# Kernel optimization log

Measured on AMD Instinct MI355X. Metric: run time of the kernel, lower is better.

Reference implementation:

```python
import jax, jax.numpy as jnp
import numpy as np

B, C, H, WID = 32, 64, 128, 128
K = 5            # co-occurrence bins (co_shape)
WH = 3           # spatial filter height/width (w_shape = (1,3,3), depth 1)
ACT_LO, ACT_HI = 0.0, 1.0  # actBounds


def setup_inputs() -> dict:
    key = jax.random.key(0)
    k1, k2, k3 = jax.random.split(key, 3)
    input_tensor = jax.random.uniform(k1, (B, C, H, WID), dtype=jnp.float32)
    # learned params: L ~ N(0, 0.1) of shape (k,k); W ~ N(0,0.1) of shape (d,h,w)
    L = 0.1 * jax.random.normal(k2, (K, K), dtype=jnp.float32)
    W = 0.1 * jax.random.normal(k3, (1, WH, WH), dtype=jnp.float32)
    return {"input_tensor": input_tensor, "W": W, "L": L}


def _quantize(x, k):
    # map activation in [ACT_LO, ACT_HI] to bin index in [0, k-1]
    b = jnp.floor((x - ACT_LO) / (ACT_HI - ACT_LO) * k)
    return jnp.clip(b, 0, k - 1).astype(jnp.int32)


def reference(input_tensor, W, L):
    """Co-occurrence layer:
    out[p] = sum_{q in 3x3 nbhd(p)} W[q-p] * L[bin(x[q]), bin(x[p])] * x[q]
    Out-of-bounds neighbors contribute 0 (zero pad => x[q]=0 kills the term),
    matching the precomputed neighbor_lookup_table boundary handling.
    """
    k = L.shape[0]
    pad = WH // 2
    bins = _quantize(input_tensor, k)                      # (B,C,H,W) int32
    xp = jnp.pad(input_tensor, ((0, 0), (0, 0), (pad, pad), (pad, pad)))
    bp = jnp.pad(bins, ((0, 0), (0, 0), (pad, pad), (pad, pad)))
    h, w = input_tensor.shape[2], input_tensor.shape[3]
    out = jnp.zeros_like(input_tensor)
    for dh in range(WH):                                   # tiny fixed 3x3 loop
        for dw in range(WH):
            xn = xp[:, :, dh:dh + h, dw:dw + w]            # shifted neighbor values
            bn = bp[:, :, dh:dh + h, dw:dw + w]            # shifted neighbor bins
            out = out + W[0, dh, dw] * L[bn, bins] * xn    # gather L + weighted acc
    return out
```

## Files before the change

### kernel.cpp

```cpp
#include <hip/hip_runtime.h>


namespace {
constexpr int H  = 128;
constexpr int WD = 128;
constexpr int PLANES = 32 * 64;
constexpr int ROWS_PER_BLOCK = 16;
constexpr int PX = 8;
constexpr int THREADS = ROWS_PER_BLOCK * (WD / PX);
constexpr int TILES = H / ROWS_PER_BLOCK;
}

__global__ __launch_bounds__(THREADS) void col_kernel(
    const float* __restrict__ x, const float* __restrict__ Wf,
    const float* __restrict__ Lf, float* __restrict__ out)
{
    __shared__ float WL[9 * 25];
    const int t = threadIdx.x;
    if (t < 225) WL[t] = Wf[t / 25] * Lf[t % 25];
    __syncthreads();

    const int plane = blockIdx.x >> 3;
    const int tile  = blockIdx.x & 7;
    const int row   = tile * ROWS_PER_BLOCK + (t >> 4);
    const int col0  = (t & 15) * PX;

    const float* xp = x + (size_t)plane * (H * WD);

    float win[3][PX + 2];
    #pragma unroll
    for (int dr = 0; dr < 3; ++dr) {
        const int rr = row + dr - 1;
        const bool vr = (rr >= 0) && (rr < H);
        const float* rp = xp + rr * WD + col0;
        float4 c0 = make_float4(0.f, 0.f, 0.f, 0.f);
        float4 c1 = make_float4(0.f, 0.f, 0.f, 0.f);
        float l = 0.f, r = 0.f;
        if (vr) {
            c0 = *(const float4*)rp;
            c1 = *(const float4*)(rp + 4);
            if (col0 > 0)       l = rp[-1];
            if (col0 < WD - PX) r = rp[PX];
        }
        win[dr][0] = l;
        win[dr][1] = c0.x; win[dr][2] = c0.y; win[dr][3] = c0.z; win[dr][4] = c0.w;
        win[dr][5] = c1.x; win[dr][6] = c1.y; win[dr][7] = c1.z; win[dr][8] = c1.w;
        win[dr][9] = r;
    }

    int bq20[3][PX + 2];
    int bp4[PX];
    #pragma unroll
    for (int dr = 0; dr < 3; ++dr) {
        #pragma unroll
        for (int j = 0; j < PX + 2; ++j) {
            int b = (int)(win[dr][j] * 5.0f);
            b = (b > 4) ? 4 : b;
            bq20[dr][j] = b * 20;
            if (dr == 1 && j >= 1 && j <= PX) bp4[j - 1] = b * 4;
        }
    }

    const char* wlb = (const char*)WL;
    float acc[PX];
    #pragma unroll
    for (int i = 0; i < PX; ++i) acc[i] = 0.f;

    #pragma unroll
    for (int dr = 0; dr < 3; ++dr) {
        #pragma unroll
        for (int dw = 0; dw < 3; ++dw) {
            #pragma unroll
            for (int i = 0; i < PX; ++i) {
                const float lw = *(const float*)(
                    wlb + (bq20[dr][i + dw] + bp4[i] + (dr * 3 + dw) * 100));
                acc[i] = fmaf(lw, win[dr][i + dw], acc[i]);
            }
        }
    }

    float* op = out + (size_t)plane * (H * WD) + row * WD + col0;
    *(float4*)op       = make_float4(acc[0], acc[1], acc[2], acc[3]);
    *(float4*)(op + 4) = make_float4(acc[4], acc[5], acc[6], acc[7]);
}

extern "C" void kernel_launch(void* const* d_in, const int* in_sizes, int n_in,
                              void* d_out, int out_size, void* d_ws, size_t ws_size,
                              hipStream_t stream) {
    const float* x  = (const float*)d_in[0];
    const float* Wf = (const float*)d_in[1];
    const float* Lf = (const float*)d_in[2];
    float* out = (float*)d_out;

    col_kernel<<<dim3(PLANES * TILES), dim3(THREADS), 0, stream>>>(x, Wf, Lf, out);
}
```

Baseline: 255.4 us.

## Compute two output rows per thread with shared window and nontemporal stores

Each thread now computes two vertically adjacent output rows, loading four input rows instead of three per row. This cuts redundant global loads of halo rows and the binning work per output. The block covers 32 rows, so each block handles a quarter plane, and launch bounds hint at 4 blocks per CU. Output writes use nontemporal vector stores to avoid polluting cache. The cost is more registers per thread, which may reduce occupancy.

```diff
diff --git a/kernel.cpp b/kernel.cpp
--- a/kernel.cpp
+++ b/kernel.cpp
@@ -5,13 +5,16 @@
 constexpr int H  = 128;
 constexpr int WD = 128;
 constexpr int PLANES = 32 * 64;
-constexpr int ROWS_PER_BLOCK = 16;
 constexpr int PX = 8;
-constexpr int THREADS = ROWS_PER_BLOCK * (WD / PX);
+constexpr int RPT = 2;
+constexpr int ROWS_PER_BLOCK = 32;
+constexpr int THREADS = (ROWS_PER_BLOCK / RPT) * (WD / PX);
 constexpr int TILES = H / ROWS_PER_BLOCK;
+
+typedef float vfloat4 __attribute__((ext_vector_type(4)));
 }
 
-__global__ __launch_bounds__(THREADS) void col_kernel(
+__global__ __launch_bounds__(THREADS, 4) void col_kernel(
     const float* __restrict__ x, const float* __restrict__ Wf,
     const float* __restrict__ Lf, float* __restrict__ out)
 {
@@ -20,17 +23,17 @@
     if (t < 225) WL[t] = Wf[t / 25] * Lf[t % 25];
     __syncthreads();
 
-    const int plane = blockIdx.x >> 3;
-    const int tile  = blockIdx.x & 7;
-    const int row   = tile * ROWS_PER_BLOCK + (t >> 4);
+    const int plane = blockIdx.x >> 2;
+    const int tile  = blockIdx.x & 3;
+    const int row0  = tile * ROWS_PER_BLOCK + (t >> 4) * RPT;
     const int col0  = (t & 15) * PX;
 
     const float* xp = x + (size_t)plane * (H * WD);
 
-    float win[3][PX + 2];
+    float win[4][PX + 2];
     #pragma unroll
-    for (int dr = 0; dr < 3; ++dr) {
-        const int rr = row + dr - 1;
+    for (int k = 0; k < 4; ++k) {
+        const int rr = row0 + k - 1;
         const bool vr = (rr >= 0) && (rr < H);
         const float* rp = xp + rr * WD + col0;
         float4 c0 = make_float4(0.f, 0.f, 0.f, 0.f);
@@ -42,46 +45,61 @@
             if (col0 > 0)       l = rp[-1];
             if (col0 < WD - PX) r = rp[PX];
         }
-        win[dr][0] = l;
-        win[dr][1] = c0.x; win[dr][2] = c0.y; win[dr][3] = c0.z; win[dr][4] = c0.w;
-        win[dr][5] = c1.x; win[dr][6] = c1.y; win[dr][7] = c1.z; win[dr][8] = c1.w;
-        win[dr][9] = r;
+        win[k][0] = l;
+        win[k][1] = c0.x; win[k][2] = c0.y; win[k][3] = c0.z; win[k][4] = c0.w;
+        win[k][5] = c1.x; win[k][6] = c1.y; win[k][7] = c1.z; win[k][8] = c1.w;
+        win[k][9] = r;
     }
 
-    int bq20[3][PX + 2];
-    int bp4[PX];
+    int bq20[4][PX + 2];
+    int bp4a[PX], bp4b[PX];
     #pragma unroll
-    for (int dr = 0; dr < 3; ++dr) {
+    for (int k = 0; k < 4; ++k) {
         #pragma unroll
         for (int j = 0; j < PX + 2; ++j) {
-            int b = (int)(win[dr][j] * 5.0f);
+            int b = (int)(win[k][j] * 5.0f);
             b = (b > 4) ? 4 : b;
-            bq20[dr][j] = b * 20;
-            if (dr == 1 && j >= 1 && j <= PX) bp4[j - 1] = b * 4;
+            bq20[k][j] = b * 20;
+            if (k == 1 && j >= 1 && j <= PX) bp4a[j - 1] = b * 4;
+            if (k == 2 && j >= 1 && j <= PX) bp4b[j - 1] = b * 4;
         }
     }
 
     const char* wlb = (const char*)WL;
-    float acc[PX];
+    float acca[PX], accb[PX];
     #pragma unroll
-    for (int i = 0; i < PX; ++i) acc[i] = 0.f;
+    for (int i = 0; i < PX; ++i) { acca[i] = 0.f; accb[i] = 0.f; }
 
     #pragma unroll
     for (int dr = 0; dr < 3; ++dr) {
         #pragma unroll
         for (int dw = 0; dw < 3; ++dw) {
+            const int imm = (dr * 3 + dw) * 100;
+            float lwa[PX], lwb[PX];
             #pragma unroll
-            for (int i = 0; i < PX; ++i) {
-                const float lw = *(const float*)(
-                    wlb + (bq20[dr][i + dw] + bp4[i] + (dr * 3 + dw) * 100));
-                acc[i] = fmaf(lw, win[dr][i + dw], acc[i]);
-            }
+            for (int i = 0; i < PX; ++i)
+                lwa[i] = *(const float*)(wlb + (bq20[dr][i + dw] + bp4a[i] + imm));
+            #pragma unroll
+            for (int i = 0; i < PX; ++i)
+                lwb[i] = *(const float*)(wlb + (bq20[dr + 1][i + dw] + bp4b[i] + imm));
+            #pragma unroll
+            for (int i = 0; i < PX; ++i)
+                acca[i] = fmaf(lwa[i], win[dr][i + dw], acca[i]);
+            #pragma unroll
+            for (int i = 0; i < PX; ++i)
+                accb[i] = fmaf(lwb[i], win[dr + 1][i + dw], accb[i]);
         }
     }
 
-    float* op = out + (size_t)plane * (H * WD) + row * WD + col0;
-    *(float4*)op       = make_float4(acc[0], acc[1], acc[2], acc[3]);
-    *(float4*)(op + 4) = make_float4(acc[4], acc[5], acc[6], acc[7]);
+    float* op = out + (size_t)plane * (H * WD) + row0 * WD + col0;
+    vfloat4 sa0 = { acca[0], acca[1], acca[2], acca[3] };
+    vfloat4 sa1 = { acca[4], acca[5], acca[6], acca[7] };
+    vfloat4 sb0 = { accb[0], accb[1], accb[2], accb[3] };
+    vfloat4 sb1 = { accb[4], accb[5], accb[6], accb[7] };
+    __builtin_nontemporal_store(sa0, (vfloat4*)op);
+    __builtin_nontemporal_store(sa1, (vfloat4*)(op + 4));
+    __builtin_nontemporal_store(sb0, (vfloat4*)(op + WD));
+    __builtin_nontemporal_store(sb1, (vfloat4*)(op + WD + 4));
 }
 
 extern "C" void kernel_launch(void* const* d_in, const int* in_sizes, int n_in,
```

New measurement: 245.4 us. 3.9% less time.

## Process eight rows per thread with a rolling register window and one block per plane

Applied to the files above, without the earlier changes.

Each block now covers a whole 128x128 plane, and each thread computes an 8-row by 8-column strip, so the grid shrinks from one block per 16-row tile to one block per plane. A rolling 4-row register window is kept and reused across output row pairs, with the next two rows prefetched before each compute step. This cuts redundant halo row loads and quantization from 3 rows per output row to about 1.25. The trade-offs are higher register pressure (launch bounds ask for 2 blocks per CU), fewer blocks to spread across the GPU, and a multiply-shift trick that derives bin*4 from bin*20.

```diff
diff --git a/kernel.cpp b/kernel.cpp
--- a/kernel.cpp
+++ b/kernel.cpp
@@ -5,13 +5,11 @@
 constexpr int H  = 128;
 constexpr int WD = 128;
 constexpr int PLANES = 32 * 64;
-constexpr int ROWS_PER_BLOCK = 16;
 constexpr int PX = 8;
-constexpr int THREADS = ROWS_PER_BLOCK * (WD / PX);
-constexpr int TILES = H / ROWS_PER_BLOCK;
+constexpr int THREADS = 256;
 }
 
-__global__ __launch_bounds__(THREADS) void col_kernel(
+__global__ __launch_bounds__(THREADS, 2) void col_kernel(
     const float* __restrict__ x, const float* __restrict__ Wf,
     const float* __restrict__ Lf, float* __restrict__ out)
 {
@@ -20,68 +18,108 @@
     if (t < 225) WL[t] = Wf[t / 25] * Lf[t % 25];
     __syncthreads();
 
-    const int plane = blockIdx.x >> 3;
-    const int tile  = blockIdx.x & 7;
-    const int row   = tile * ROWS_PER_BLOCK + (t >> 4);
-    const int col0  = (t & 15) * PX;
+    const int col0 = (t & 15) * PX;
+    const int r0   = (t >> 4) * 8;
 
-    const float* xp = x + (size_t)plane * (H * WD);
+    const float* xp = x + (size_t)blockIdx.x * (H * WD);
+    float* opb      = out + (size_t)blockIdx.x * (H * WD);
+    const char* wlb = (const char*)WL;
 
-    float win[3][PX + 2];
-    #pragma unroll
-    for (int dr = 0; dr < 3; ++dr) {
-        const int rr = row + dr - 1;
-        const bool vr = (rr >= 0) && (rr < H);
-        const float* rp = xp + rr * WD + col0;
-        float4 c0 = make_float4(0.f, 0.f, 0.f, 0.f);
-        float4 c1 = make_float4(0.f, 0.f, 0.f, 0.f);
-        float l = 0.f, r = 0.f;
-        if (vr) {
-            c0 = *(const float4*)rp;
-            c1 = *(const float4*)(rp + 4);
-            if (col0 > 0)       l = rp[-1];
-            if (col0 < WD - PX) r = rp[PX];
-        }
-        win[dr][0] = l;
-        win[dr][1] = c0.x; win[dr][2] = c0.y; win[dr][3] = c0.z; win[dr][4] = c0.w;
-        win[dr][5] = c1.x; win[dr][6] = c1.y; win[dr][7] = c1.z; win[dr][8] = c1.w;
-        win[dr][9] = r;
+    float win[4][PX + 2];
+    int   bq[4][PX + 2];
+    float n0[PX + 2], n1[PX + 2];
+
+#define LOAD_ROW(DST, RR) {                                               \
+    const int _rr = (RR);                                                 \
+    if (_rr >= 0 && _rr < H) {                                            \
+        const float* _rp = xp + _rr * WD + col0;                          \
+        const float4 _c0 = *(const float4*)_rp;          \
+        const float4 _c1 = *(const float4*)(_rp + 4);                     \
+        DST[0] = (col0 > 0) ? _rp[-1] : 0.f;                              \
+        DST[1] = _c0.x; DST[2] = _c0.y; DST[3] = _c0.z; DST[4] = _c0.w;   \
+        DST[5] = _c1.x; DST[6] = _c1.y; DST[7] = _c1.z; DST[8] = _c1.w;   \
+        DST[9] = (col0 < WD - PX) ? _rp[PX] : 0.f;                        \
+    } else {                                                              \
+        _Pragma("unroll")                                                 \
+        for (int _j = 0; _j < PX + 2; ++_j) DST[_j] = 0.f;                \
+    } }
+
+#define QUANT_ROW(S) {                                                    \
+    _Pragma("unroll")                                                     \
+    for (int _j = 0; _j < PX + 2; ++_j) {                                 \
+        int _b = (int)(win[S][_j] * 5.0f);        \
+        _b = (_b > 4) ? 4 : _b;                                           \
+        bq[S][_j] = _b * 20;                                              \
+    } }
+
+#define RETIRE(S, SRC) {                                                  \
+    _Pragma("unroll")                                                     \
+    for (int _j = 0; _j < PX + 2; ++_j) win[S][_j] = SRC[_j];             \
+    QUANT_ROW(S) }
+
+#define TERMS(QS, DR, BP, ACC) {                                          \
+    _Pragma("unroll")                                                     \
+    for (int _dw = 0; _dw < 3; ++_dw) {                                   \
+        float _lw[PX];                                                    \
+        _Pragma("unroll")                                                 \
+        for (int _i = 0; _i < PX; ++_i)                                   \
+            _lw[_i] = *(const float*)(wlb +                               \
+                (bq[QS][_i + _dw] + BP[_i] + ((DR) * 3 + _dw) * 100));    \
+        _Pragma("unroll")                                                 \
+        for (int _i = 0; _i < PX; ++_i)                                   \
+            ACC[_i] = fmaf(_lw[_i], win[QS][_i + _dw], ACC[_i]);          \
+    } }
+
+#define COMPUTE2(PA, PB, PC, PD, R) {                                     \
+    int bp4a[PX], bp4b[PX];                                               \
+    _Pragma("unroll")                                                     \
+    for (int _i = 0; _i < PX; ++_i) {                                     \
+        bp4a[_i] = (bq[PB][_i + 1] * 52429) >> 18;       \
+        bp4b[_i] = (bq[PC][_i + 1] * 52429) >> 18;                        \
+    }                                                                     \
+    float acca[PX], accb[PX];                                             \
+    _Pragma("unroll")                                                     \
+    for (int _i = 0; _i < PX; ++_i) { acca[_i] = 0.f; accb[_i] = 0.f; }   \
+    TERMS(PA, 0, bp4a, acca)                                              \
+    TERMS(PB, 0, bp4b, accb)                                              \
+    TERMS(PB, 1, bp4a, acca)                                              \
+    TERMS(PC, 1, bp4b, accb)                                              \
+    TERMS(PC, 2, bp4a, acca)                                              \
+    TERMS(PD, 2, bp4b, accb)                                              \
+    float* _op = opb + (R) * WD + col0;                                   \
+    *(float4*)_op            = make_float4(acca[0], acca[1], acca[2], acca[3]); \
+    *(float4*)(_op + 4)      = make_float4(acca[4], acca[5], acca[6], acca[7]); \
+    *(float4*)(_op + WD)     = make_float4(accb[0], accb[1], accb[2], accb[3]); \
+    *(float4*)(_op + WD + 4) = make_float4(accb[4], accb[5], accb[6], accb[7]); \
     }
 
-    int bq20[3][PX + 2];
-    int bp4[PX];
-    #pragma unroll
-    for (int dr = 0; dr < 3; ++dr) {
-        #pragma unroll
-        for (int j = 0; j < PX + 2; ++j) {
-            int b = (int)(win[dr][j] * 5.0f);
-            b = (b > 4) ? 4 : b;
-            bq20[dr][j] = b * 20;
-            if (dr == 1 && j >= 1 && j <= PX) bp4[j - 1] = b * 4;
-        }
-    }
+    LOAD_ROW(win[0], r0 - 1) QUANT_ROW(0)
+    LOAD_ROW(win[1], r0 + 0) QUANT_ROW(1)
+    LOAD_ROW(win[2], r0 + 1) QUANT_ROW(2)
+    LOAD_ROW(win[3], r0 + 2) QUANT_ROW(3)
 
-    const char* wlb = (const char*)WL;
-    float acc[PX];
-    #pragma unroll
-    for (int i = 0; i < PX; ++i) acc[i] = 0.f;
+    LOAD_ROW(n0, r0 + 3)
+    LOAD_ROW(n1, r0 + 4)
+    COMPUTE2(0, 1, 2, 3, r0)
+    RETIRE(0, n0) RETIRE(1, n1)
 
-    #pragma unroll
-    for (int dr = 0; dr < 3; ++dr) {
-        #pragma unroll
-        for (int dw = 0; dw < 3; ++dw) {
-            #pragma unroll
-            for (int i = 0; i < PX; ++i) {
-                const float lw = *(const float*)(
-                    wlb + (bq20[dr][i + dw] + bp4[i] + (dr * 3 + dw) * 100));
-                acc[i] = fmaf(lw, win[dr][i + dw], acc[i]);
-            }
-        }
-    }
+    LOAD_ROW(n0, r0 + 5)
+    LOAD_ROW(n1, r0 + 6)
+    COMPUTE2(2, 3, 0, 1, r0 + 2)
+    RETIRE(2, n0) RETIRE(3, n1)
 
-    float* op = out + (size_t)plane * (H * WD) + row * WD + col0;
-    *(float4*)op       = make_float4(acc[0], acc[1], acc[2], acc[3]);
-    *(float4*)(op + 4) = make_float4(acc[4], acc[5], acc[6], acc[7]);
+    LOAD_ROW(n0, r0 + 7)
+    LOAD_ROW(n1, r0 + 8)
+    COMPUTE2(0, 1, 2, 3, r0 + 4)
+    RETIRE(0, n0) RETIRE(1, n1)
+
+    COMPUTE2(2, 3, 0, 1, r0 + 6)
+
+#undef LOAD_ROW
+#undef QUANT_ROW
+#undef RETIRE
+#undef TERMS
+#undef COMPUTE2
 }
 
 extern "C" void kernel_launch(void* const* d_in, const int* in_sizes, int n_in,
@@ -92,5 +130,5 @@
     const float* Lf = (const float*)d_in[2];
     float* out = (float*)d_out;
 
-    col_kernel<<<dim3(PLANES * TILES), dim3(THREADS), 0, stream>>>(x, Wf, Lf, out);
+    col_kernel<<<dim3(PLANES), dim3(THREADS), 0, stream>>>(x, Wf, Lf, out);
 }
```

New measurement: 252.2 us. About the same (-1.3%).
